# Optimization experiments

Measured on AMD Instinct MI355X. Metric: run time of the kernel, lower is better.

The kernel has to match this reference:

```python
import jax, jax.numpy as jnp
import numpy as np

N_NODES = 50000
N_EDGES = 800000
IN_FEATS = 128
N_HEADS = 4
OUT_FEATS = 32
NEG_SLOPE = 0.01  # F.leaky_relu default


def setup_inputs() -> dict:
    key = jax.random.key(0)
    k1, k2, k3, k4, k5, k6 = jax.random.split(key, 6)
    feat = jax.random.normal(k1, (N_NODES, IN_FEATS), dtype=jnp.float32)
    src = jax.random.randint(k2, (N_EDGES,), 0, N_NODES, dtype=jnp.int64)
    dst = jax.random.randint(k3, (N_EDGES,), 0, N_NODES, dtype=jnp.int64)
    # xavier-ish scaled params
    W_fc = jax.random.normal(k4, (IN_FEATS, N_HEADS * OUT_FEATS), dtype=jnp.float32) * 0.1
    attn_l = jax.random.normal(k5, (N_HEADS, OUT_FEATS), dtype=jnp.float32) * 0.1
    attn_r = jax.random.normal(k6, (N_HEADS, OUT_FEATS), dtype=jnp.float32) * 0.1
    return {"feat": feat, "src": src, "dst": dst, "W_fc": W_fc,
            "attn_l": attn_l, "attn_r": attn_r}


def reference(feat, src, dst, W_fc, attn_l, attn_r):
    N = feat.shape[0]
    H, D = attn_l.shape
    # fc projection -> [N, H, D]
    h = (feat @ W_fc).reshape(N, H, D)
    # per-node attention logits [N, H]
    el = jnp.einsum('nhd,hd->nh', h, attn_l)
    er = jnp.einsum('nhd,hd->nh', h, attn_r)
    # edge scores: u_add_v then leaky_relu -> [E, H]
    e = jax.nn.leaky_relu(el[src] + er[dst], NEG_SLOPE)
    # faithful to torch.softmax(e, dim=1): softmax over the HEADS axis per edge
    a = jax.nn.softmax(e, axis=1)
    # weighted messages and sum-aggregation over destination nodes
    msg = h[src] * a[:, :, None]                     # [E, H, D]
    rst = jax.ops.segment_sum(msg, dst, num_segments=N)  # [N, H, D]
    # residual: res_fc is Identity since in_feats == H*D
    rst = rst + feat.reshape(N, H, D)
    return jax.nn.elu(rst)
```

## Files before the change

kernel.cpp:

```cpp
#include <hip/hip_runtime.h>

typedef float f32x4 __attribute__((ext_vector_type(4)));
typedef __bf16 bf16x8 __attribute__((ext_vector_type(8)));
typedef unsigned short u16x4 __attribute__((ext_vector_type(4)));
typedef unsigned short u16x8 __attribute__((ext_vector_type(8)));

#define BSH 5
#define BN 32
#define CAPFIX 1024
#define PNB_MAX 1600
#define PCH 4096

__device__ inline unsigned short f2bf(float x) {
  unsigned int u = __builtin_bit_cast(unsigned int, x);
  unsigned int r = (u + 0x7FFFu + ((u >> 16) & 1u)) >> 16;
  return (unsigned short)r;
}
__device__ inline float bf2f(unsigned short h) {
  unsigned int u = ((unsigned int)h) << 16;
  return __builtin_bit_cast(float, u);
}

#define FC_ROWS 64
__global__ __launch_bounds__(256) void fc_mfma(const float* __restrict__ feat,
                                               const float* __restrict__ W,
                                               const float* __restrict__ al,
                                               const float* __restrict__ ar,
                                               unsigned short* __restrict__ hbf,
                                               float* __restrict__ el,
                                               float* __restrict__ er, int N) {
  __shared__ unsigned short Wbl[16 * 128 * 8];
  __shared__ unsigned short Albs[16 * 64 * 8];
  int t = threadIdx.x;
  int row0 = blockIdx.x * FC_ROWS;
#pragma unroll
  for (int i = 0; i < 8; ++i) {
    int ch = i * 256 + t;
    int col = ch & 127;
    int kg = ch >> 7;
    float v[8];
#pragma unroll
    for (int j = 0; j < 8; ++j) v[j] = W[(kg * 8 + j) * 128 + col];
    int scol = col ^ ((kg & 7) << 4);
    u16x8 pk = {f2bf(v[0]), f2bf(v[1]), f2bf(v[2]), f2bf(v[3]),
                f2bf(v[4]), f2bf(v[5]), f2bf(v[6]), f2bf(v[7])};
    *(u16x8*)&Wbl[(size_t)(kg * 128 + scol) * 8] = pk;
  }
#pragma unroll
  for (int i = 0; i < 4; ++i) {
    int ch = i * 256 + t;
    int row = ch >> 4;
    int kg = ch & 15;
    int grow = row0 + row;
    f32x4 x0 = {}, x1 = {};
    if (grow < N) {
      const f32x4* fp = (const f32x4*)(feat + (size_t)grow * 128 + kg * 8);
      x0 = fp[0];
      x1 = fp[1];
    }
    int sc = kg * 64 + (row ^ kg);
    u16x8 pk = {f2bf(x0[0]), f2bf(x0[1]), f2bf(x0[2]), f2bf(x0[3]),
                f2bf(x1[0]), f2bf(x1[1]), f2bf(x1[2]), f2bf(x1[3])};
    *(u16x8*)&Albs[sc * 8] = pk;
  }
  __syncthreads();
  int w = t >> 6;
  int l = t & 63;
  int lr = l & 15;
  int lhi = l >> 4;
  f32x4 acc[8] = {};
  bf16x8 afr[4];
#pragma unroll
  for (int ks = 0; ks < 4; ++ks) {
    int kg = ks * 4 + lhi;
    int row = w * 16 + lr;
    afr[ks] = *(const bf16x8*)&Albs[(kg * 64 + (row ^ kg)) * 8];
  }
#pragma unroll
  for (int nt = 0; nt < 8; ++nt) {
#pragma unroll
    for (int ks = 0; ks < 4; ++ks) {
      int kg = ks * 4 + lhi;
      int col = nt * 16 + lr;
      int scol = col ^ ((kg & 7) << 4);
      bf16x8 b = *(const bf16x8*)&Wbl[(size_t)(kg * 128 + scol) * 8];
      acc[nt] = __builtin_amdgcn_mfma_f32_16x16x32_bf16(afr[ks], b, acc[nt], 0, 0, 0);
    }
  }
#pragma unroll
  for (int nt = 0; nt < 8; ++nt) {
#pragma unroll
    for (int r = 0; r < 4; ++r) {
      int g = row0 + w * 16 + lhi * 4 + r;
      if (g < N) hbf[(size_t)g * 128 + nt * 16 + lr] = f2bf(acc[nt][r]);
    }
  }
  f32x4 pl[4] = {}, pr[4] = {};
#pragma unroll
  for (int nt = 0; nt < 8; ++nt) {
    int hd = nt >> 1;
    float wl = al[nt * 16 + lr];
    float wr = ar[nt * 16 + lr];
#pragma unroll
    for (int r = 0; r < 4; ++r) {
      pl[r][hd] += acc[nt][r] * wl;
      pr[r][hd] += acc[nt][r] * wr;
    }
  }
#pragma unroll
  for (int off = 1; off < 16; off <<= 1) {
#pragma unroll
    for (int r = 0; r < 4; ++r) {
#pragma unroll
      for (int c = 0; c < 4; ++c) {
        pl[r][c] += __shfl_xor(pl[r][c], off);
        pr[r][c] += __shfl_xor(pr[r][c], off);
      }
    }
  }
  if (lr == 0) {
#pragma unroll
    for (int r = 0; r < 4; ++r) {
      int g = row0 + w * 16 + lhi * 4 + r;
      if (g < N) *(f32x4*)(el + (size_t)g * 4) = pl[r];
    }
  } else if (lr == 1) {
#pragma unroll
    for (int r = 0; r < 4; ++r) {
      int g = row0 + w * 16 + lhi * 4 + r;
      if (g < N) *(f32x4*)(er + (size_t)g * 4) = pr[r];
    }
  }
}

__global__ __launch_bounds__(256) void partition_kernel(const int* __restrict__ src,
                                                        const int* __restrict__ dst,
                                                        int* __restrict__ bcursor,
                                                        int* __restrict__ tmp,
                                                        int E, int nbuck) {
  __shared__ int cnt[PNB_MAX];
  __shared__ int lcur[PNB_MAX];
  int t = threadIdx.x;
  int base = blockIdx.x * PCH;
  for (int i = t; i < nbuck; i += 256) cnt[i] = 0;
  __syncthreads();
  int rec[16];
  int bb[16];
#pragma unroll
  for (int i = 0; i < 16; ++i) {
    int e = base + t + i * 256;
    bb[i] = -1;
    if (e < E) {
      int d = dst[e];
      int b = d >> BSH;
      bb[i] = b;
      rec[i] = (src[e] & 0xFFFF) | ((d & (BN - 1)) << 16);
      atomicAdd(&cnt[b], 1);
    }
  }
  __syncthreads();
  for (int i = t; i < nbuck; i += 256) {
    int c = cnt[i];
    lcur[i] = c ? atomicAdd(&bcursor[i], c) : 0;
  }
  __syncthreads();
#pragma unroll
  for (int i = 0; i < 16; ++i) {
    if (bb[i] >= 0) {
      int p = atomicAdd(&lcur[bb[i]], 1);
      if (p < CAPFIX) tmp[(size_t)bb[i] * CAPFIX + p] = rec[i];
    }
  }
}

__global__ __launch_bounds__(256) void bucket_gather(const unsigned short* __restrict__ hbf,
                                                     const float* __restrict__ el,
                                                     const float* __restrict__ er,
                                                     const int* __restrict__ bcnt,
                                                     const int* __restrict__ tmp,
                                                     const float* __restrict__ feat,
                                                     float* __restrict__ out, int N) {
  __shared__ unsigned short as_s[CAPFIX];
  __shared__ unsigned short as_a[CAPFIX * 4];
  __shared__ f32x4 er_l[BN];
  __shared__ int cnt[BN], lb[BN], lc2[BN];
  int t = threadIdx.x;
  int bkt = blockIdx.x;
  int nstart = bkt << BSH;
  if (t < BN) {
    int nd = nstart + t;
    f32x4 e4 = {};
    if (nd < N) e4 = *(const f32x4*)(er + (size_t)nd * 4);
    er_l[t] = e4;
    cnt[t] = 0;
    lc2[t] = 0;
  }
  __syncthreads();
  int nrec = min(bcnt[bkt], CAPFIX);
  int myrec[4], mydlo[4];
#pragma unroll
  for (int i = 0; i < 4; ++i) {
    int idx = t + i * 256;
    mydlo[i] = -1;
    if (idx < nrec) {
      int r = tmp[(size_t)bkt * CAPFIX + idx];
      myrec[i] = r;
      int dlo = (r >> 16) & (BN - 1);
      mydlo[i] = dlo;
      atomicAdd(&cnt[dlo], 1);
    }
  }
  __syncthreads();
  if (t < BN) {
    int v = cnt[t];
    int s = v;
#pragma unroll
    for (int o = 1; o < BN; o <<= 1) {
      int x = __shfl_up(s, o, BN);
      if (t >= o) s += x;
    }
    lb[t] = s - v;
  }
  __syncthreads();
#pragma unroll
  for (int i = 0; i < 4; ++i) {
    if (mydlo[i] >= 0) {
      int r = myrec[i];
      int s = r & 0xFFFF;
      int dlo = mydlo[i];
      int p = lb[dlo] + atomicAdd(&lc2[dlo], 1);
      f32x4 l4 = *(const f32x4*)(el + (size_t)s * 4);
      f32x4 r4 = er_l[dlo];
      float e0 = l4[0] + r4[0];
      float e1 = l4[1] + r4[1];
      float e2 = l4[2] + r4[2];
      float e3 = l4[3] + r4[3];
      e0 = e0 > 0.f ? e0 : 0.01f * e0;
      e1 = e1 > 0.f ? e1 : 0.01f * e1;
      e2 = e2 > 0.f ? e2 : 0.01f * e2;
      e3 = e3 > 0.f ? e3 : 0.01f * e3;
      float m = fmaxf(fmaxf(e0, e1), fmaxf(e2, e3));
      float a0 = __expf(e0 - m);
      float a1 = __expf(e1 - m);
      float a2 = __expf(e2 - m);
      float a3 = __expf(e3 - m);
      float inv = 1.0f / (a0 + a1 + a2 + a3);
      u16x4 a = {f2bf(a0 * inv), f2bf(a1 * inv), f2bf(a2 * inv), f2bf(a3 * inv)};
      as_s[p] = (unsigned short)s;
      *(u16x4*)&as_a[p * 4] = a;
    }
  }
  __syncthreads();
  int gid = t >> 5, lane = t & 31, head = lane >> 3;
#pragma unroll
  for (int ni = 0; ni < 4; ++ni) {
    int g = gid * 4 + ni;
    int nd = nstart + g;
    f32x4 acc = {};
    int st = lb[g], en = st + cnt[g];
    int e = st;
    for (; e + 3 < en; e += 4) {
      int s0 = as_s[e + 0];
      int s1 = as_s[e + 1];
      int s2 = as_s[e + 2];
      int s3 = as_s[e + 3];
      float a0 = bf2f(as_a[(e + 0) * 4 + head]);
      float a1 = bf2f(as_a[(e + 1) * 4 + head]);
      float a2 = bf2f(as_a[(e + 2) * 4 + head]);
      float a3 = bf2f(as_a[(e + 3) * 4 + head]);
      u16x4 v0 = *(const u16x4*)&hbf[(size_t)s0 * 128 + lane * 4];
      u16x4 v1 = *(const u16x4*)&hbf[(size_t)s1 * 128 + lane * 4];
      u16x4 v2 = *(const u16x4*)&hbf[(size_t)s2 * 128 + lane * 4];
      u16x4 v3 = *(const u16x4*)&hbf[(size_t)s3 * 128 + lane * 4];
      f32x4 h0 = {bf2f(v0[0]), bf2f(v0[1]), bf2f(v0[2]), bf2f(v0[3])};
      f32x4 h1 = {bf2f(v1[0]), bf2f(v1[1]), bf2f(v1[2]), bf2f(v1[3])};
      f32x4 h2 = {bf2f(v2[0]), bf2f(v2[1]), bf2f(v2[2]), bf2f(v2[3])};
      f32x4 h3 = {bf2f(v3[0]), bf2f(v3[1]), bf2f(v3[2]), bf2f(v3[3])};
      acc += h0 * a0;
      acc += h1 * a1;
      acc += h2 * a2;
      acc += h3 * a3;
    }
    for (; e < en; ++e) {
      int s0 = as_s[e];
      float a0 = bf2f(as_a[e * 4 + head]);
      u16x4 v0 = *(const u16x4*)&hbf[(size_t)s0 * 128 + lane * 4];
      f32x4 h0 = {bf2f(v0[0]), bf2f(v0[1]), bf2f(v0[2]), bf2f(v0[3])};
      acc += h0 * a0;
    }
    if (nd < N) {
      f32x4 f = *(const f32x4*)(feat + (size_t)nd * 128 + lane * 4);
      f32x4 o = acc + f;
#pragma unroll
      for (int c = 0; c < 4; ++c) o[c] = o[c] > 0.f ? o[c] : expm1f(o[c]);
      *(f32x4*)(out + (size_t)nd * 128 + lane * 4) = o;
    }
  }
}

extern "C" void kernel_launch(void* const* d_in, const int* in_sizes, int n_in,
                              void* d_out, int out_size, void* d_ws, size_t ws_size,
                              hipStream_t stream) {
  const float* feat = (const float*)d_in[0];
  const int* src = (const int*)d_in[1];
  const int* dst = (const int*)d_in[2];
  const float* W = (const float*)d_in[3];
  const float* al = (const float*)d_in[4];
  const float* ar = (const float*)d_in[5];
  float* out = (float*)d_out;

  int N = in_sizes[0] / 128;
  int E = in_sizes[1];
  int nbuck = (N + BN - 1) >> BSH;

  char* p = (char*)d_ws;
  unsigned short* hbf = (unsigned short*)p; p += (size_t)N * 128 * 2;
  float* el = (float*)p; p += (size_t)N * 4 * 4;
  float* er = (float*)p; p += (size_t)N * 4 * 4;
  int* bcursor = (int*)p; p += (size_t)((nbuck + 3) & ~3) * 4;
  int* tmp = (int*)p;

  hipMemsetAsync(bcursor, 0, (size_t)nbuck * sizeof(int), stream);
  partition_kernel<<<(E + PCH - 1) / PCH, 256, 0, stream>>>(src, dst, bcursor, tmp, E, nbuck);
  fc_mfma<<<(N + FC_ROWS - 1) / FC_ROWS, 256, 0, stream>>>(feat, W, al, ar, hbf, el, er, N);
  bucket_gather<<<nbuck, 256, 0, stream>>>(hbf, el, er, bcursor, tmp, feat, out, N);
}
```

Measured before the change: 84.38 us.

## Fuse edge partition and FC projection into one heterogeneous launch

Merges the partition kernel and the MFMA projection kernel into a single launch. Blocks below npart do edge bucketing and the rest do the FC projection, sharing one 48KB shared-memory buffer. The hipMemsetAsync is also replaced by a small zero kernel. The aim is to cut launch overhead and let the two independent stages run concurrently on the GPU. In exchange, every block reserves the larger shared-memory footprint, which may lower occupancy for the partition blocks.

```diff
diff --git a/kernel.cpp b/kernel.cpp
--- a/kernel.cpp
+++ b/kernel.cpp
@@ -10,6 +10,7 @@
 #define CAPFIX 1024
 #define PNB_MAX 1600
 #define PCH 4096
+#define FC_ROWS 64
 
 __device__ inline unsigned short f2bf(float x) {
   unsigned int u = __builtin_bit_cast(unsigned int, x);
@@ -21,18 +22,60 @@
   return __builtin_bit_cast(float, u);
 }
 
-#define FC_ROWS 64
-__global__ __launch_bounds__(256) void fc_mfma(const float* __restrict__ feat,
-                                               const float* __restrict__ W,
-                                               const float* __restrict__ al,
-                                               const float* __restrict__ ar,
-                                               unsigned short* __restrict__ hbf,
-                                               float* __restrict__ el,
-                                               float* __restrict__ er, int N) {
-  __shared__ unsigned short Wbl[16 * 128 * 8];
-  __shared__ unsigned short Albs[16 * 64 * 8];
+__global__ __launch_bounds__(256) void zero_kernel(int* __restrict__ p, int n) {
+  int i = blockIdx.x * 256 + threadIdx.x;
+  if (i < n) p[i] = 0;
+}
+
+__device__ void partition_body(char* smem, const int* __restrict__ src,
+                               const int* __restrict__ dst,
+                               int* __restrict__ bcursor, int* __restrict__ tmp,
+                               int E, int nbuck, int blk) {
+  int* cnt = (int*)smem;
+  int* lcur = cnt + PNB_MAX;
   int t = threadIdx.x;
-  int row0 = blockIdx.x * FC_ROWS;
+  int base = blk * PCH;
+  for (int i = t; i < nbuck; i += 256) cnt[i] = 0;
+  __syncthreads();
+  int rec[16];
+  int bb[16];
+#pragma unroll
+  for (int i = 0; i < 16; ++i) {
+    int e = base + t + i * 256;
+    bb[i] = -1;
+    if (e < E) {
+      int d = dst[e];
+      int b = d >> BSH;
+      bb[i] = b;
+      rec[i] = (src[e] & 0xFFFF) | ((d & (BN - 1)) << 16);
+      atomicAdd(&cnt[b], 1);
+    }
+  }
+  __syncthreads();
+  for (int i = t; i < nbuck; i += 256) {
+    int c = cnt[i];
+    lcur[i] = c ? atomicAdd(&bcursor[i], c) : 0;
+  }
+  __syncthreads();
+#pragma unroll
+  for (int i = 0; i < 16; ++i) {
+    if (bb[i] >= 0) {
+      int p = atomicAdd(&lcur[bb[i]], 1);
+      if (p < CAPFIX) tmp[(size_t)bb[i] * CAPFIX + p] = rec[i];
+    }
+  }
+}
+
+__device__ void fc_body(char* smem, const float* __restrict__ feat,
+                        const float* __restrict__ W,
+                        const float* __restrict__ al, const float* __restrict__ ar,
+                        unsigned short* __restrict__ hbf,
+                        float* __restrict__ el, float* __restrict__ er,
+                        int N, int blk) {
+  unsigned short* Wbl = (unsigned short*)smem;
+  unsigned short* Albs = (unsigned short*)(smem + 32768);
+  int t = threadIdx.x;
+  int row0 = blk * FC_ROWS;
 #pragma unroll
   for (int i = 0; i < 8; ++i) {
     int ch = i * 256 + t;
@@ -133,44 +176,23 @@
   }
 }
 
-__global__ __launch_bounds__(256) void partition_kernel(const int* __restrict__ src,
-                                                        const int* __restrict__ dst,
-                                                        int* __restrict__ bcursor,
-                                                        int* __restrict__ tmp,
-                                                        int E, int nbuck) {
-  __shared__ int cnt[PNB_MAX];
-  __shared__ int lcur[PNB_MAX];
-  int t = threadIdx.x;
-  int base = blockIdx.x * PCH;
-  for (int i = t; i < nbuck; i += 256) cnt[i] = 0;
-  __syncthreads();
-  int rec[16];
-  int bb[16];
-#pragma unroll
-  for (int i = 0; i < 16; ++i) {
-    int e = base + t + i * 256;
-    bb[i] = -1;
-    if (e < E) {
-      int d = dst[e];
-      int b = d >> BSH;
-      bb[i] = b;
-      rec[i] = (src[e] & 0xFFFF) | ((d & (BN - 1)) << 16);
-      atomicAdd(&cnt[b], 1);
-    }
-  }
-  __syncthreads();
-  for (int i = t; i < nbuck; i += 256) {
-    int c = cnt[i];
-    lcur[i] = c ? atomicAdd(&bcursor[i], c) : 0;
-  }
-  __syncthreads();
-#pragma unroll
-  for (int i = 0; i < 16; ++i) {
-    if (bb[i] >= 0) {
-      int p = atomicAdd(&lcur[bb[i]], 1);
-      if (p < CAPFIX) tmp[(size_t)bb[i] * CAPFIX + p] = rec[i];
-    }
-  }
+__global__ __launch_bounds__(256) void fused_pfc(const int* __restrict__ src,
+                                                 const int* __restrict__ dst,
+                                                 int* __restrict__ bcursor,
+                                                 int* __restrict__ tmp,
+                                                 const float* __restrict__ feat,
+                                                 const float* __restrict__ W,
+                                                 const float* __restrict__ al,
+                                                 const float* __restrict__ ar,
+                                                 unsigned short* __restrict__ hbf,
+                                                 float* __restrict__ el,
+                                                 float* __restrict__ er,
+                                                 int E, int N, int nbuck, int npart) {
+  __shared__ alignas(16) char smem[49152];
+  if ((int)blockIdx.x < npart)
+    partition_body(smem, src, dst, bcursor, tmp, E, nbuck, blockIdx.x);
+  else
+    fc_body(smem, feat, W, al, ar, hbf, el, er, N, blockIdx.x - npart);
 }
 
 __global__ __launch_bounds__(256) void bucket_gather(const unsigned short* __restrict__ hbf,
@@ -320,8 +342,11 @@
   int* bcursor = (int*)p; p += (size_t)((nbuck + 3) & ~3) * 4;
   int* tmp = (int*)p;
 
-  hipMemsetAsync(bcursor, 0, (size_t)nbuck * sizeof(int), stream);
-  partition_kernel<<<(E + PCH - 1) / PCH, 256, 0, stream>>>(src, dst, bcursor, tmp, E, nbuck);
-  fc_mfma<<<(N + FC_ROWS - 1) / FC_ROWS, 256, 0, stream>>>(feat, W, al, ar, hbf, el, er, N);
+  int npart = (E + PCH - 1) / PCH;
+  int nfc = (N + FC_ROWS - 1) / FC_ROWS;
+
+  zero_kernel<<<(nbuck + 255) / 256, 256, 0, stream>>>(bcursor, nbuck);
+  fused_pfc<<<npart + nfc, 256, 0, stream>>>(src, dst, bcursor, tmp, feat, W, al, ar,
+                                             hbf, el, er, E, N, nbuck, npart);
   bucket_gather<<<nbuck, 256, 0, stream>>>(hbf, el, er, bcursor, tmp, feat, out, N);
 }
```

Result: faster. 71.54 us (-15.2%).
